# Kernel tuning notes

Measured on AMD Instinct MI355X. Metric: run time of the kernel, lower is better.

## Reference

```python
import jax, jax.numpy as jnp
import numpy as np

B, N, M, U, L = 2048, 256, 128, 512, 2   # batch, memory locations, memory width, num_units, num_layers
RH, WH, SH = 2, 2, 1                      # read heads, write heads, conv_shift_range
CLIP = 20.0
HEAD_R = M + 3 + (2 * SH + 1)             # 134 = k(M)+beta+g+s(2r+1)+gamma
HEAD_W = HEAD_R + 2 * M                   # 390 = + erase(M) + add(M)


def setup_inputs():
    key = jax.random.key(0)
    ks = jax.random.split(key, 12)
    def nrm(k, shape, s=0.05):
        return jax.random.normal(k, shape, jnp.float32) * s
    return {
        "X": jax.random.normal(ks[0], (B, U), jnp.float32),
        "m0": nrm(ks[1], (1, N, M), 0.5),
        "H0": nrm(ks[2], (L, 1, U)),
        "C0": nrm(ks[3], (L, 1, U)),
        "R0": nrm(ks[4], (RH, 1, M)),
        "A0": nrm(ks[5], (RH + WH, 1, N)),
        "W_prep": nrm(ks[6], (M * RH, U)),
        "b_prep": jnp.zeros((U,), jnp.float32),
        "W_lstm": nrm(ks[7], (L, 3 * U, 4 * U)),
        "b_lstm": jnp.zeros((L, 4 * U), jnp.float32),
        "W_r": nrm(ks[8], (U, RH * HEAD_R)),
        "b_r": jnp.zeros((RH * HEAD_R,), jnp.float32),
        "W_w": nrm(ks[9], (U, WH * HEAD_W)),
        "b_w": jnp.zeros((WH * HEAD_W,), jnp.float32),
        "W_ou": nrm(ks[10], (U + RH * M, U)),
        "b_ou": jnp.zeros((U,), jnp.float32),
    }


def _addressing(k, beta, g, s, gamma, m, a_prev):
    # k [B,M], beta/g/gamma [B], s [B,2*SH+1], m [B,N,M], a_prev [B,N]
    inner = jnp.einsum('bnm,bm->bn', m, k)
    k_norm = jnp.sqrt(jnp.sum(k * k, axis=1, keepdims=True))   # [B,1]
    m_norm = jnp.sqrt(jnp.sum(m * m, axis=2))                  # [B,N]
    K = inner / (k_norm * m_norm + 1e-8)
    w_c = jax.nn.softmax(beta[:, None] * K, axis=1)            # exp/sum in source == softmax
    w_g = g[:, None] * w_c + (1.0 - g[:, None]) * a_prev
    # The stacked-slice s_matrix in the source is exactly circular convolution:
    # w_conv[i] = sum_d s_d * w_g[(i - d) mod N], d in {0..SH, -SH..-1} matching s layout.
    shifts = list(range(0, SH + 1)) + list(range(-SH, 0))
    w_conv = sum(s[:, j:j + 1] * jnp.roll(w_g, shifts[j], axis=1) for j in range(2 * SH + 1))
    w_sharp = w_conv ** gamma[:, None]
    return w_sharp / jnp.sum(w_sharp, axis=1, keepdims=True)


def reference(X, m0, H0, C0, R0, A0, W_prep, b_prep, W_lstm, b_lstm,
              W_r, b_r, W_w, b_w, W_ou, b_ou):
    b = X.shape[0]
    m = jnp.broadcast_to(m0, (b, N, M))
    R_prev = [jnp.broadcast_to(jnp.tanh(R0[i]), (b, M)) for i in range(RH)]
    A_prev = [jnp.broadcast_to(jax.nn.softmax(A0[i], axis=-1), (b, N)) for i in range(RH + WH)]

    # controller
    h = jnp.concatenate(R_prev, axis=1) @ W_prep + b_prep
    for l in range(L):
        x_in = jnp.concatenate([X, h], axis=1)                              # [B,2U]
        h_prev = jnp.broadcast_to(H0[l], (b, U))
        c_prev = jnp.broadcast_to(C0[l], (b, U))
        z = jnp.concatenate([x_in, h_prev], axis=1) @ W_lstm[l] + b_lstm[l]  # [B,4U]
        i_g, f_g, g_g, o_g = jnp.split(z, 4, axis=1)
        c = jax.nn.sigmoid(f_g) * c_prev + jax.nn.sigmoid(i_g) * jnp.tanh(g_g)
        h = jax.nn.sigmoid(o_g) * jnp.tanh(c)
    h = jnp.clip(h, -CLIP, CLIP)

    r_heads = (h @ W_r + b_r).reshape(b, RH, HEAD_R)
    w_heads = (h @ W_w + b_w).reshape(b, WH, HEAD_W)
    heads = [r_heads[:, i] for i in range(RH)] + [w_heads[:, i] for i in range(WH)]

    A_t = []
    for ii, hd in enumerate(heads):
        A_t.append(_addressing(
            k=jnp.tanh(hd[:, :M]),
            beta=jax.nn.softplus(hd[:, M]),
            g=jax.nn.sigmoid(hd[:, M + 1]),
            s=jax.nn.softmax(hd[:, M + 2:M + 2 + 2 * SH + 1], axis=-1),
            gamma=jax.nn.softplus(hd[:, M + 2 + 2 * SH + 1]),
            m=m, a_prev=A_prev[ii]))

    # reads from old memory
    R_t = [jnp.einsum('bn,bnm->bm', A_t[i], m) for i in range(RH)]

    # sequential erase/add writes
    m_t = m
    for ii in range(WH):
        w = A_t[RH + ii][:, :, None]                                  # [B,N,1]
        del_v = jax.nn.sigmoid(w_heads[:, ii, -2 * M:-M])[:, None, :]  # [B,1,M]
        add_v = jnp.tanh(w_heads[:, ii, -M:])[:, None, :]
        m_t = m_t * (1.0 - w * del_v) + w * add_v

    y = jnp.clip(jnp.concatenate([h] + R_t, axis=1) @ W_ou + b_ou, -CLIP, CLIP)
    return y, m_t
```

## Files before the change

### kernel.cpp

```cpp
#include <hip/hip_runtime.h>
#include <math.h>

static constexpr int Bn = 2048;
static constexpr int Nn = 256;
static constexpr int Mn = 128;
static constexpr int Un = 512;

static constexpr size_t OFF_MNORM = 4608;
static constexpr size_t OFF_APREV = 4864;
static constexpr size_t OFF_BIASH = 5888;
static constexpr size_t OFF_KMAT  = 16384;
static constexpr size_t OFF_HEADS = OFF_KMAT + (size_t)8192 * 256;
static constexpr size_t OFF_AT    = OFF_HEADS + (size_t)2048 * 1048;
static constexpr size_t OFF_ERA   = OFF_AT + (size_t)2 * 2048 * 256;
static constexpr size_t OFF_ADD   = OFF_ERA + (size_t)2048 * 256;
static constexpr size_t OFF_XHB   = OFF_ADD + (size_t)2048 * 256;
static constexpr size_t OFF_HCAT  = OFF_XHB + 524288;
static constexpr size_t OFF_W0T   = OFF_HCAT + 524288;
static constexpr size_t OFF_W1T   = OFF_W0T + 524288;
static constexpr size_t OFF_WRWT  = OFF_W1T + 1048576;
static constexpr size_t OFF_WCOMB = OFF_WRWT + 294912;
static constexpr size_t OFF_WR2T  = OFF_WCOMB + 262144;
static constexpr size_t OFF_M0B   = OFF_WR2T + 65536;
static constexpr size_t OFF_ZPART = OFF_M0B + 16384 + 524288;

static constexpr int S_X0  = 0;
static constexpr int S_M0  = 512;
static constexpr int S_W0  = 528;
static constexpr int S_W1  = 1552;
static constexpr int S_WR  = 3600;
static constexpr int S_WW  = 3744;
static constexpr int S_WOU = 4144;
static constexpr int S_WR2 = 4400;
static constexpr int S_CA  = 4528;
static constexpr int S_ZC  = 4529;
static constexpr int S_END = 4657;

#define DEV __device__ __forceinline__

typedef __attribute__((ext_vector_type(8))) short bf16x8;
typedef __attribute__((ext_vector_type(4))) float f32x4;
typedef __attribute__((ext_vector_type(8))) unsigned short ushort8;
typedef unsigned int u32;

DEV float sigf(float x) { return 1.0f / (1.0f + expf(-x)); }
DEV float softplusf(float x) { return x > 20.0f ? x : log1pf(expf(x)); }
DEV unsigned short f2bf(float f) {
    unsigned u = __float_as_uint(f);
    u = (u + 0x7FFFu + ((u >> 16) & 1u)) >> 16;
    return (unsigned short)u;
}
DEV void gload16(const unsigned short* g, unsigned short* l) {
    __builtin_amdgcn_global_load_lds(
        (const __attribute__((address_space(1))) u32*)g,
        (__attribute__((address_space(3))) u32*)l, 16, 0, 0);
}

DEV float blk_reduce_max(float v, float* red) {
    int tid = threadIdx.x;
    red[tid] = v; __syncthreads();
    for (int s = (int)blockDim.x >> 1; s > 0; s >>= 1) {
        if (tid < s) red[tid] = fmaxf(red[tid], red[tid + s]);
        __syncthreads();
    }
    float r = red[0]; __syncthreads();
    return r;
}
DEV float blk_reduce_sum(float v, float* red) {
    int tid = threadIdx.x;
    red[tid] = v; __syncthreads();
    for (int s = (int)blockDim.x >> 1; s > 0; s >>= 1) {
        if (tid < s) red[tid] += red[tid + s];
        __syncthreads();
    }
    float r = red[0]; __syncthreads();
    return r;
}

#define GEMM_STAGE(buf, k0)                                                     \
    {                                                                           \
        _Pragma("unroll")                                                       \
        for (int q = 0; q < 2; ++q)                                             \
            gload16(A  + (size_t)(row0 + q * 32 + (tid >> 3)) * lda + (k0) + ke,\
                    &As[buf][q * 2048 + tid * 8]);                              \
        _Pragma("unroll")                                                       \
        for (int q = 0; q < 4; ++q)                                             \
            gload16(Wt + (size_t)(col0 + q * 32 + (tid >> 3)) * ldw + (k0) + ke,\
                    &Ws[buf][q * 2048 + tid * 8]);                              \
    }

#define GEMM_PROLOG                                                             \
    __shared__ __align__(16) unsigned short As[2][64 * 64];                     \
    __shared__ __align__(16) unsigned short Ws[2][128 * 64];                    \
    const int tid  = threadIdx.x;                                               \
    const int lane = tid & 63;                                                  \
    const int wave = tid >> 6;                                                  \
    const int wr = wave >> 1, wc = wave & 1;                                    \
    const int row0 = blockIdx.x * 64;                                           \
    const int col0 = blockIdx.y * 128;                                          \
    const int ke = ((tid & 7) * 8) ^ (((tid >> 3) & 7) << 3);                   \
    const int frow = lane & 15;                                                 \
    const int fko  = (lane >> 4) * 8;                                           \
    const int fxm  = (frow & 7) << 3;                                           \
    f32x4 acc[2][4];                                                            \
    _Pragma("unroll")                                                           \
    for (int i = 0; i < 2; ++i)                                                 \
        _Pragma("unroll")                                                       \
        for (int j = 0; j < 4; ++j) acc[i][j] = (f32x4){0.f, 0.f, 0.f, 0.f};

#define GEMM_FRAGS_AND_MFMA(Ab, Wb)                                             \
    {                                                                           \
        bf16x8 af[2][2], wf[2][4];                                              \
        _Pragma("unroll")                                                       \
        for (int kk = 0; kk < 2; ++kk) {                                        \
            _Pragma("unroll")                                                   \
            for (int i = 0; i < 2; ++i) {                                       \
                int fr = wr * 32 + i * 16 + frow;                               \
                af[kk][i] = *(const bf16x8*)&(Ab)[fr * 64 + ((kk * 32 + fko) ^ fxm)]; \
            }                                                                   \
            _Pragma("unroll")                                                   \
            for (int j = 0; j < 4; ++j) {                                       \
                int fr = wc * 64 + j * 16 + frow;                               \
                wf[kk][j] = *(const bf16x8*)&(Wb)[fr * 64 + ((kk * 32 + fko) ^ fxm)]; \
            }                                                                   \
        }                                                                       \
        __builtin_amdgcn_s_setprio(1);                                          \
        _Pragma("unroll")                                                       \
        for (int kk = 0; kk < 2; ++kk)                                          \
            _Pragma("unroll")                                                   \
            for (int i = 0; i < 2; ++i)                                         \
                _Pragma("unroll")                                               \
                for (int j = 0; j < 4; ++j)                                     \
                    acc[i][j] = __builtin_amdgcn_mfma_f32_16x16x32_bf16(        \
                        af[kk][i], wf[kk][j], acc[i][j], 0, 0, 0);              \
        __builtin_amdgcn_s_setprio(0);                                          \
    }

#define GEMM_MAINLOOP(Kr)                                                       \
    {                                                                           \
        const int nt = (Kr) >> 6;                                               \
        int cur = 0;                                                            \
        GEMM_STAGE(0, 0);                                                       \
        for (int t = 0; t < nt; ++t) {                                          \
            __syncthreads();                                                    \
            if (t + 1 < nt) GEMM_STAGE(cur ^ 1, (t + 1) * 64);                  \
            GEMM_FRAGS_AND_MFMA(As[cur], Ws[cur]);                              \
            cur ^= 1;                                                           \
        }                                                                       \
    }

__global__ __launch_bounds__(256) void gemm_bf16(
    const unsigned short* __restrict__ A, int lda,
    const unsigned short* __restrict__ Wt, int ldw,
    const float* __restrict__ bias,
    float* __restrict__ C, unsigned short* __restrict__ Cb, int ldc,
    int Nr, int Kr, int epi)
{
    GEMM_PROLOG
    GEMM_MAINLOOP(Kr)
    #pragma unroll
    for (int i = 0; i < 2; ++i) {
        int m0r = row0 + wr * 32 + i * 16 + (lane >> 4) * 4;
        #pragma unroll
        for (int j = 0; j < 4; ++j) {
            int n = col0 + wc * 64 + j * 16 + (lane & 15);
            if (n >= Nr) continue;
            float bv = bias ? bias[n] : 0.f;
            #pragma unroll
            for (int r = 0; r < 4; ++r) {
                float v = acc[i][j][r] + bv;
                if (epi == 1) v = fminf(fmaxf(v, -20.f), 20.f);
                if (epi == 2) Cb[(size_t)(m0r + r) * ldc + n] = f2bf(v);
                else          C [(size_t)(m0r + r) * ldc + n] = v;
            }
        }
    }
}

__global__ __launch_bounds__(256) void gemm_pfold(
    const unsigned short* __restrict__ WR2T,
    const unsigned short* __restrict__ M0B,
    unsigned short* __restrict__ WCOMB)
{
    const unsigned short* A  = WR2T + blockIdx.z * 128;
    const unsigned short* Wt = M0B;
    const int lda = 256, ldw = 128;
    unsigned short* Cb = WCOMB + 512 + blockIdx.z * 256;
    GEMM_PROLOG
    GEMM_MAINLOOP(128)
    #pragma unroll
    for (int i = 0; i < 2; ++i) {
        int m0r = row0 + wr * 32 + i * 16 + (lane >> 4) * 4;
        #pragma unroll
        for (int j = 0; j < 4; ++j) {
            int n = col0 + wc * 64 + j * 16 + (lane & 15);
            #pragma unroll
            for (int r = 0; r < 4; ++r)
                Cb[(size_t)(m0r + r) * 1024 + n] = f2bf(acc[i][j][r]);
        }
    }
}

__global__ __launch_bounds__(256) void gemm_lstm(
    const unsigned short* __restrict__ A, int lda,
    const unsigned short* __restrict__ Wt, int ldw,
    const float* __restrict__ zpart, const float* __restrict__ b_lstm,
    int z, const float* __restrict__ c0,
    unsigned short* __restrict__ hout, int ldh, int Kr, int doclip)
{
    GEMM_PROLOG
    GEMM_MAINLOOP(Kr)
    const int uu = lane & 15;
    const int q  = (col0 >> 6) + wc;
    const int uq = q * 16 + uu;
    const float c0v = c0[uq];
    float bg[4];
    #pragma unroll
    for (int g = 0; g < 4; ++g) {
        int j = g * 512 + q * 16 + uu;
        float a = b_lstm[z * 2048 + j];
        #pragma unroll
        for (int p = 0; p < 8; ++p)
            a += zpart[((size_t)z * 8 + p) * 2048 + j];
        bg[g] = a;
    }
    #pragma unroll
    for (int i = 0; i < 2; ++i) {
        int rbase = row0 + wr * 32 + i * 16 + (lane >> 4) * 4;
        #pragma unroll
        for (int r = 0; r < 4; ++r) {
            float ig = acc[i][0][r] + bg[0];
            float fg = acc[i][1][r] + bg[1];
            float gg = acc[i][2][r] + bg[2];
            float og = acc[i][3][r] + bg[3];
            float c = sigf(fg) * c0v + sigf(ig) * tanhf(gg);
            float h = sigf(og) * tanhf(c);
            if (doclip) h = fminf(fmaxf(h, -20.f), 20.f);
            hout[(size_t)(rbase + r) * ldh + uq] = f2bf(h);
        }
    }
}

__global__ __launch_bounds__(256) void gemm_kmat(
    const float* __restrict__ heads,
    const unsigned short* __restrict__ M0B,
    float* __restrict__ C)
{
    __shared__ __align__(16) unsigned short As[2][64 * 64];
    __shared__ __align__(16) unsigned short Ws[2][128 * 64];
    const int tid  = threadIdx.x;
    const int lane = tid & 63;
    const int wave = tid >> 6;
    const int wr = wave >> 1, wc = wave & 1;
    const int row0 = blockIdx.x * 64;
    const int col0 = blockIdx.y * 128;
    const int ke = ((tid & 7) * 8) ^ (((tid >> 3) & 7) << 3);
    const int frow = lane & 15;
    const int fko  = (lane >> 4) * 8;
    const int fxm  = (frow & 7) << 3;
    f32x4 acc[2][4];
    #pragma unroll
    for (int i = 0; i < 2; ++i)
        #pragma unroll
        for (int j = 0; j < 4; ++j) acc[i][j] = (f32x4){0.f, 0.f, 0.f, 0.f};

#define KMAT_STAGE(buf, k0)                                                     \
    {                                                                           \
        _Pragma("unroll")                                                       \
        for (int q = 0; q < 2; ++q) {                                           \
            int R = row0 + q * 32 + (tid >> 3);                                 \
            int b = R >> 2, ih = R & 3;                                         \
            int cb = (ih < 2) ? ih * 134 : 268 + (ih - 2) * 390;                \
            const float* hp = heads + (size_t)b * 1048 + cb + (k0) + ke;        \
            ushort8 o;                                                          \
            _Pragma("unroll")                                                   \
            for (int j = 0; j < 8; ++j) o[j] = f2bf(tanhf(hp[j]));              \
            *(ushort8*)&As[buf][q * 2048 + tid * 8] = o;                        \
        }                                                                       \
        _Pragma("unroll")                                                       \
        for (int q = 0; q < 4; ++q)                                             \
            gload16(M0B + (size_t)(col0 + q * 32 + (tid >> 3)) * 128 + (k0) + ke,\
                    &Ws[buf][q * 2048 + tid * 8]);                              \
    }

    int cur = 0;
    KMAT_STAGE(0, 0);
    for (int t = 0; t < 2; ++t) {
        __syncthreads();
        if (t == 0) KMAT_STAGE(1, 64);
        GEMM_FRAGS_AND_MFMA(As[cur], Ws[cur]);
        cur ^= 1;
    }
#undef KMAT_STAGE
    #pragma unroll
    for (int i = 0; i < 2; ++i) {
        int m0r = row0 + wr * 32 + i * 16 + (lane >> 4) * 4;
        #pragma unroll
        for (int j = 0; j < 4; ++j) {
            int n = col0 + wc * 64 + j * 16 + (lane & 15);
            #pragma unroll
            for (int r = 0; r < 4; ++r)
                C[(size_t)(m0r + r) * 256 + n] = acc[i][j][r];
        }
    }
}

DEV void dev_cvt8(const float* src, int lds, unsigned short* dst, int ldd,
                  int c8, int bloc, int tid)
{
    size_t idx = (size_t)bloc * 256 + tid;
    size_t r = idx / c8, c = (idx % c8) * 8;
    const float* s = src + r * lds + c;
    float4 v0 = *(const float4*)s;
    float4 v1 = *(const float4*)(s + 4);
    ushort8 o;
    o[0] = f2bf(v0.x); o[1] = f2bf(v0.y); o[2] = f2bf(v0.z); o[3] = f2bf(v0.w);
    o[4] = f2bf(v1.x); o[5] = f2bf(v1.y); o[6] = f2bf(v1.z); o[7] = f2bf(v1.w);
    *(ushort8*)(dst + r * ldd + c) = o;
}

DEV void dev_cvtT(const float* src, int R, int C, int lds,
                  unsigned short* dst, int ldd, int mode, int bx, int by,
                  int tid, float* t )
{
    const int x = tid & 31;
    for (int y = tid >> 5; y < 32; y += 8) {
        int r = by * 32 + y, c = bx * 32 + x;
        int scol = c;
        if (mode) scol = ((c >> 4) & 3) * 512 + (c >> 6) * 16 + (c & 15);
        t[y * 33 + x] = (r < R && c < C) ? src[(size_t)r * lds + scol] : 0.f;
    }
    __syncthreads();
    for (int y = tid >> 5; y < 32; y += 8) {
        int c = bx * 32 + y, r = by * 32 + x;
        if (c < C && r < R) dst[(size_t)c * ldd + r] = f2bf(t[x * 33 + y]);
    }
}

__global__ __launch_bounds__(256) void k_prep(
    const float* __restrict__ X, const float* __restrict__ m0,
    const float* __restrict__ H0, const float* __restrict__ R0,
    const float* __restrict__ A0, const float* __restrict__ W_prep,
    const float* __restrict__ b_prep, const float* __restrict__ W_lstm,
    const float* __restrict__ W_r, const float* __restrict__ b_r,
    const float* __restrict__ W_w, const float* __restrict__ b_w,
    const float* __restrict__ W_ou, float* __restrict__ ws)
{
    __shared__ float sh[32 * 33 + 64];
    const int bid = blockIdx.x, tid = threadIdx.x;
    unsigned short* XHB   = (unsigned short*)(ws + OFF_XHB);
    unsigned short* W0T   = (unsigned short*)(ws + OFF_W0T);
    unsigned short* W1T   = (unsigned short*)(ws + OFF_W1T);
    unsigned short* WRWT  = (unsigned short*)(ws + OFF_WRWT);
    unsigned short* WCOMB = (unsigned short*)(ws + OFF_WCOMB);
    unsigned short* WR2T  = (unsigned short*)(ws + OFF_WR2T);
    unsigned short* M0B   = (unsigned short*)(ws + OFF_M0B);

    if (bid < S_M0) {
        dev_cvt8(X, 512, XHB, 1024, 64, bid - S_X0, tid);
    } else if (bid < S_W0) {
        dev_cvt8(m0, 128, M0B, 128, 16, bid - S_M0, tid);
    } else if (bid < S_W1) {
        int s = bid - S_W0;
        dev_cvtT(W_lstm, 512, 2048, 2048, W0T, 512, 1, s & 63, s >> 6, tid, sh);
    } else if (bid < S_WR) {
        int s = bid - S_W1;
        dev_cvtT(W_lstm + (size_t)1536 * 2048, 1024, 2048, 2048, W1T, 1024, 1,
                 s & 63, s >> 6, tid, sh);
    } else if (bid < S_WW) {
        int s = bid - S_WR;
        dev_cvtT(W_r, 512, 268, 268, WRWT, 512, 0, s % 9, s / 9, tid, sh);
    } else if (bid < S_WOU) {
        int s = bid - S_WW;
        dev_cvtT(W_w, 512, 780, 780, WRWT + (size_t)268 * 512, 512, 0,
                 s % 25, s / 25, tid, sh);
    } else if (bid < S_WR2) {
        int s = bid - S_WOU;
        dev_cvtT(W_ou, 512, 512, 512, WCOMB, 1024, 0, s & 15, s >> 4, tid, sh);
    } else if (bid < S_CA) {
        int s = bid - S_WR2;
        dev_cvtT(W_ou + (size_t)512 * 512, 256, 512, 512, WR2T, 256, 0,
                 s & 15, s >> 4, tid, sh);
    } else if (bid < S_ZC) {
        float* red = sh;
        for (int i = 0; i < 4; ++i) {
            float v = A0[i * 256 + tid];
            float mx = blk_reduce_max(v, red);
            float e = expf(v - mx);
            float s = blk_reduce_sum(e, red);
            ws[OFF_APREV + i * 256 + tid] = e / s;
        }
        float acc = 0.f;
        for (int m = 0; m < 128; ++m) {
            float t = m0[(size_t)tid * 128 + m];
            acc = fmaf(t, t, acc);
        }
        ws[OFF_MNORM + tid] = sqrtf(acc);
        for (int j = tid; j < 1152; j += 256)
            ws[OFF_BIASH + j] = (j < 268) ? b_r[j] : (j < 1048 ? b_w[j - 268] : 0.f);
    } else {
        int sub = bid - S_ZC;
        int colb = sub & 7, up = (sub >> 3) & 7, z = sub >> 6;
        int j = colb * 256 + tid;
        float acc = 0.f;
        if (z == 0) {
            if (up < 4) {
                sh[256 + tid] = tanhf(R0[tid]);
                __syncthreads();
                if (tid < 128) {
                    int u = up * 128 + tid;
                    float a = b_prep[u];
                    for (int k = 0; k < 256; ++k)
                        a = fmaf(sh[256 + k], W_prep[(size_t)k * 512 + u], a);
                    sh[tid] = a;
                }
                __syncthreads();
                const int u0 = up * 128;
                #pragma unroll 4
                for (int t = 0; t < 128; ++t)
                    acc = fmaf(sh[t], W_lstm[(size_t)(512 + u0 + t) * 2048 + j], acc);
            } else {
                const int u0 = up * 128;
                #pragma unroll 4
                for (int t = 0; t < 128; ++t)
                    acc = fmaf(H0[u0 - 512 + t],
                               W_lstm[(size_t)(512 + u0 + t) * 2048 + j], acc);
            }
        } else {
            const int u0 = up * 64;
            const float* W1 = W_lstm + (size_t)1536 * 2048;
            #pragma unroll 4
            for (int t = 0; t < 64; ++t)
                acc = fmaf(H0[512 + u0 + t], W1[(size_t)(1024 + u0 + t) * 2048 + j], acc);
        }
        (ws + OFF_ZPART)[((size_t)z * 8 + up) * 2048 + j] = acc;
    }
}

__global__ __launch_bounds__(256) void k_addr(
    const float* __restrict__ heads, const float* __restrict__ kmat,
    const float* __restrict__ mnorm, const float* __restrict__ aprev,
    float* __restrict__ at, unsigned short* __restrict__ hcat,
    float* __restrict__ era, float* __restrict__ addv)
{
    __shared__ float red[256];
    __shared__ float wgs[256];
    __shared__ float sc[6];
    const int b = blockIdx.x, i = blockIdx.y, tid = threadIdx.x;
    const int cb = (i < 2) ? i * 134 : 268 + (i - 2) * 390;
    const float* hd = heads + (size_t)b * 1048 + cb;
    float kv = (tid < 128) ? tanhf(hd[tid]) : 0.f;
    float ksq = blk_reduce_sum(kv * kv, red);
    float kn = sqrtf(ksq);
    if (i >= 2 && tid < 128) {
        era [((size_t)b * 2 + (i - 2)) * 128 + tid] = sigf(hd[134 + tid]);
        addv[((size_t)b * 2 + (i - 2)) * 128 + tid] = tanhf(hd[262 + tid]);
    }
    if (tid == 0) {
        sc[0] = softplusf(hd[128]);
        sc[1] = sigf(hd[129]);
        float v0 = hd[130], v1 = hd[131], v2 = hd[132];
        float mx = fmaxf(v0, fmaxf(v1, v2));
        float e0 = expf(v0 - mx), e1 = expf(v1 - mx), e2 = expf(v2 - mx);
        float ssum = e0 + e1 + e2;
        sc[2] = e0 / ssum; sc[3] = e1 / ssum; sc[4] = e2 / ssum;
        sc[5] = softplusf(hd[133]);
    }
    __syncthreads();
    const float beta = sc[0], g = sc[1], s0 = sc[2], s1 = sc[3], s2 = sc[4],
                gamma = sc[5];
    float inner = kmat[((size_t)b * 4 + i) * 256 + tid];
    float K = inner / (kn * mnorm[tid] + 1e-8f);
    float x = beta * K;
    float mx = blk_reduce_max(x, red);
    float e = expf(x - mx);
    float se = blk_reduce_sum(e, red);
    float wc = e / se;
    float wg = g * wc + (1.f - g) * aprev[i * 256 + tid];
    wgs[tid] = wg;
    __syncthreads();
    float wconv = s0 * wg + s1 * wgs[(tid + 255) & 255] + s2 * wgs[(tid + 1) & 255];
    float wsh = powf(wconv, gamma);
    float ssum = blk_reduce_sum(wsh, red);
    float w = wsh / ssum;
    if (i < 2) hcat[(size_t)b * 1024 + 512 + i * 256 + tid] = f2bf(w);
    else       at[((size_t)(i - 2) * Bn + b) * 256 + tid] = w;
}

__global__ void k_mem(const float* __restrict__ m0, const float* __restrict__ at,
                      const float* __restrict__ era, const float* __restrict__ addv,
                      float* __restrict__ outm)
{
    const size_t total = (size_t)Bn * Nn * (Mn / 4);
    for (size_t idx = (size_t)blockIdx.x * blockDim.x + threadIdx.x;
         idx < total; idx += (size_t)gridDim.x * blockDim.x) {
        int mq = (int)(idx & 31);
        int n  = (int)((idx >> 5) & 255);
        int b  = (int)(idx >> 13);
        float4 t  = reinterpret_cast<const float4*>(m0)[n * 32 + mq];
        float w0 = at[((size_t)0 * Bn + b) * 256 + n];
        float w1 = at[((size_t)1 * Bn + b) * 256 + n];
        float4 e0 = reinterpret_cast<const float4*>(era) [((size_t)b * 2 + 0) * 32 + mq];
        float4 a0 = reinterpret_cast<const float4*>(addv)[((size_t)b * 2 + 0) * 32 + mq];
        float4 e1 = reinterpret_cast<const float4*>(era) [((size_t)b * 2 + 1) * 32 + mq];
        float4 a1 = reinterpret_cast<const float4*>(addv)[((size_t)b * 2 + 1) * 32 + mq];
#define UPD(c) { t.c = t.c * (1.f - w0 * e0.c) + w0 * a0.c; \
                 t.c = t.c * (1.f - w1 * e1.c) + w1 * a1.c; }
        UPD(x) UPD(y) UPD(z) UPD(w)
#undef UPD
        reinterpret_cast<float4*>(outm)[idx] = t;
    }
}

extern "C" void kernel_launch(void* const* d_in, const int* in_sizes, int n_in,
                              void* d_out, int out_size, void* d_ws, size_t ws_size,
                              hipStream_t stream)
{
    const float* X      = (const float*)d_in[0];
    const float* m0     = (const float*)d_in[1];
    const float* H0     = (const float*)d_in[2];
    const float* C0     = (const float*)d_in[3];
    const float* R0     = (const float*)d_in[4];
    const float* A0     = (const float*)d_in[5];
    const float* W_prep = (const float*)d_in[6];
    const float* b_prep = (const float*)d_in[7];
    const float* W_lstm = (const float*)d_in[8];
    const float* b_lstm = (const float*)d_in[9];
    const float* W_r    = (const float*)d_in[10];
    const float* b_r    = (const float*)d_in[11];
    const float* W_w    = (const float*)d_in[12];
    const float* b_w    = (const float*)d_in[13];
    const float* W_ou   = (const float*)d_in[14];
    const float* b_ou   = (const float*)d_in[15];
    float* ws  = (float*)d_ws;
    float* out = (float*)d_out;

    unsigned short* XHB   = (unsigned short*)(ws + OFF_XHB);
    unsigned short* HCAT  = (unsigned short*)(ws + OFF_HCAT);
    unsigned short* W0T   = (unsigned short*)(ws + OFF_W0T);
    unsigned short* W1T   = (unsigned short*)(ws + OFF_W1T);
    unsigned short* WRWT  = (unsigned short*)(ws + OFF_WRWT);
    unsigned short* WCOMB = (unsigned short*)(ws + OFF_WCOMB);
    unsigned short* WR2T  = (unsigned short*)(ws + OFF_WR2T);
    unsigned short* M0B   = (unsigned short*)(ws + OFF_M0B);

    k_prep<<<S_END, 256, 0, stream>>>(
        X, m0, H0, R0, A0, W_prep, b_prep, W_lstm, W_r, b_r, W_w, b_w, W_ou, ws);

    gemm_pfold<<<dim3(8, 2, 2), 256, 0, stream>>>(WR2T, M0B, WCOMB);

    gemm_lstm<<<dim3(32, 16), 256, 0, stream>>>(
        XHB, 1024, W0T, 512, ws + OFF_ZPART, b_lstm, 0, C0, XHB + 512, 1024, 512, 0);
    gemm_lstm<<<dim3(32, 16), 256, 0, stream>>>(
        XHB, 1024, W1T, 1024, ws + OFF_ZPART, b_lstm, 1, C0 + 512, HCAT, 1024, 1024, 1);

    gemm_bf16<<<dim3(32, 9), 256, 0, stream>>>(
        HCAT, 1024, WRWT, 512, ws + OFF_BIASH, ws + OFF_HEADS, nullptr, 1048, 1048, 512, 0);

    gemm_kmat<<<dim3(128, 2), 256, 0, stream>>>(
        ws + OFF_HEADS, M0B, ws + OFF_KMAT);

    k_addr<<<dim3(Bn, 4), 256, 0, stream>>>(
        ws + OFF_HEADS, ws + OFF_KMAT, ws + OFF_MNORM, ws + OFF_APREV,
        ws + OFF_AT, HCAT, ws + OFF_ERA, ws + OFF_ADD);

    gemm_bf16<<<dim3(32, 4), 256, 0, stream>>>(
        HCAT, 1024, WCOMB, 1024, b_ou, out, nullptr, 512, 512, 1024, 1);

    k_mem<<<2048, 256, 0, stream>>>(
        m0, ws + OFF_AT, ws + OFF_ERA, ws + OFF_ADD, out + (size_t)Bn * Un);
}
```

Measured before the change: 205.7 us.

## Fuse write-head addressing into memory update kernel and rework GEMM barriers

The write-head addressing (erase/add vectors and attention weights) now runs inside the memory-update kernel, one block per batch row, and the results stay in shared memory. This removes the global round trip for at/era/add and shrinks k_addr to the two read heads. The GEMM main loop also swaps its single __syncthreads for explicit vmcnt waits and two s_barriers per iteration, so the next tile's global loads can stay in flight during the MFMA work. In exchange, the memory-update blocks do a serial addressing phase before streaming, and the extra barrier adds sync cost.

```diff
diff --git a/kernel.cpp b/kernel.cpp
--- a/kernel.cpp
+++ b/kernel.cpp
@@ -11,10 +11,7 @@
 static constexpr size_t OFF_BIASH = 5888;
 static constexpr size_t OFF_KMAT  = 16384;
 static constexpr size_t OFF_HEADS = OFF_KMAT + (size_t)8192 * 256;
-static constexpr size_t OFF_AT    = OFF_HEADS + (size_t)2048 * 1048;
-static constexpr size_t OFF_ERA   = OFF_AT + (size_t)2 * 2048 * 256;
-static constexpr size_t OFF_ADD   = OFF_ERA + (size_t)2048 * 256;
-static constexpr size_t OFF_XHB   = OFF_ADD + (size_t)2048 * 256;
+static constexpr size_t OFF_XHB   = OFF_HEADS + (size_t)2048 * 1048;
 static constexpr size_t OFF_HCAT  = OFF_XHB + 524288;
 static constexpr size_t OFF_W0T   = OFF_HCAT + 524288;
 static constexpr size_t OFF_W1T   = OFF_W0T + 524288;
@@ -142,9 +139,18 @@
         int cur = 0;                                                            \
         GEMM_STAGE(0, 0);                                                       \
         for (int t = 0; t < nt; ++t) {                                          \
-            __syncthreads();                                                    \
-            if (t + 1 < nt) GEMM_STAGE(cur ^ 1, (t + 1) * 64);                  \
+            if (t + 1 < nt) {                                                   \
+                GEMM_STAGE(cur ^ 1, (t + 1) * 64);                              \
+                asm volatile("s_waitcnt vmcnt(6)" ::: "memory");                \
+            } else {                                                            \
+                asm volatile("s_waitcnt vmcnt(0)" ::: "memory");                \
+            }                                                                   \
+            __builtin_amdgcn_sched_barrier(0);                                  \
+            __builtin_amdgcn_s_barrier();                                       \
+            __builtin_amdgcn_sched_barrier(0);                                  \
             GEMM_FRAGS_AND_MFMA(As[cur], Ws[cur]);                              \
+            __builtin_amdgcn_sched_barrier(0);                                  \
+            __builtin_amdgcn_s_barrier();                                       \
             cur ^= 1;                                                           \
         }                                                                       \
     }
@@ -440,22 +446,15 @@
 __global__ __launch_bounds__(256) void k_addr(
     const float* __restrict__ heads, const float* __restrict__ kmat,
     const float* __restrict__ mnorm, const float* __restrict__ aprev,
-    float* __restrict__ at, unsigned short* __restrict__ hcat,
-    float* __restrict__ era, float* __restrict__ addv)
+    unsigned short* __restrict__ hcat)
 {
     __shared__ float red[256];
     __shared__ float wgs[256];
     __shared__ float sc[6];
     const int b = blockIdx.x, i = blockIdx.y, tid = threadIdx.x;
-    const int cb = (i < 2) ? i * 134 : 268 + (i - 2) * 390;
-    const float* hd = heads + (size_t)b * 1048 + cb;
+    const float* hd = heads + (size_t)b * 1048 + i * 134;
     float kv = (tid < 128) ? tanhf(hd[tid]) : 0.f;
-    float ksq = blk_reduce_sum(kv * kv, red);
-    float kn = sqrtf(ksq);
-    if (i >= 2 && tid < 128) {
-        era [((size_t)b * 2 + (i - 2)) * 128 + tid] = sigf(hd[134 + tid]);
-        addv[((size_t)b * 2 + (i - 2)) * 128 + tid] = tanhf(hd[262 + tid]);
-    }
+    float kn = sqrtf(blk_reduce_sum(kv * kv, red));
     if (tid == 0) {
         sc[0] = softplusf(hd[128]);
         sc[1] = sigf(hd[129]);
@@ -482,33 +481,76 @@
     float wconv = s0 * wg + s1 * wgs[(tid + 255) & 255] + s2 * wgs[(tid + 1) & 255];
     float wsh = powf(wconv, gamma);
     float ssum = blk_reduce_sum(wsh, red);
-    float w = wsh / ssum;
-    if (i < 2) hcat[(size_t)b * 1024 + 512 + i * 256 + tid] = f2bf(w);
-    else       at[((size_t)(i - 2) * Bn + b) * 256 + tid] = w;
-}
-
-__global__ void k_mem(const float* __restrict__ m0, const float* __restrict__ at,
-                      const float* __restrict__ era, const float* __restrict__ addv,
-                      float* __restrict__ outm)
-{
-    const size_t total = (size_t)Bn * Nn * (Mn / 4);
-    for (size_t idx = (size_t)blockIdx.x * blockDim.x + threadIdx.x;
-         idx < total; idx += (size_t)gridDim.x * blockDim.x) {
-        int mq = (int)(idx & 31);
-        int n  = (int)((idx >> 5) & 255);
-        int b  = (int)(idx >> 13);
-        float4 t  = reinterpret_cast<const float4*>(m0)[n * 32 + mq];
-        float w0 = at[((size_t)0 * Bn + b) * 256 + n];
-        float w1 = at[((size_t)1 * Bn + b) * 256 + n];
-        float4 e0 = reinterpret_cast<const float4*>(era) [((size_t)b * 2 + 0) * 32 + mq];
-        float4 a0 = reinterpret_cast<const float4*>(addv)[((size_t)b * 2 + 0) * 32 + mq];
-        float4 e1 = reinterpret_cast<const float4*>(era) [((size_t)b * 2 + 1) * 32 + mq];
-        float4 a1 = reinterpret_cast<const float4*>(addv)[((size_t)b * 2 + 1) * 32 + mq];
+    hcat[(size_t)b * 1024 + 512 + i * 256 + tid] = f2bf(wsh / ssum);
+}
+
+__global__ __launch_bounds__(256) void k_mem(
+    const float* __restrict__ m0, const float* __restrict__ heads,
+    const float* __restrict__ kmat, const float* __restrict__ mnorm,
+    const float* __restrict__ aprev, float* __restrict__ outm)
+{
+    __shared__ float red[256];
+    __shared__ float wgs[256];
+    __shared__ float sc[6];
+    __shared__ __align__(16) float at_s[2][256];
+    __shared__ __align__(16) float er_s[2][128];
+    __shared__ __align__(16) float ad_s[2][128];
+    const int b = blockIdx.x, tid = threadIdx.x;
+
+    for (int ii = 0; ii < 2; ++ii) {
+        const int i = 2 + ii;
+        const float* hd = heads + (size_t)b * 1048 + 268 + ii * 390;
+        float kv = (tid < 128) ? tanhf(hd[tid]) : 0.f;
+        float kn = sqrtf(blk_reduce_sum(kv * kv, red));
+        if (tid < 128) {
+            er_s[ii][tid] = sigf(hd[134 + tid]);
+            ad_s[ii][tid] = tanhf(hd[262 + tid]);
+        }
+        if (tid == 0) {
+            sc[0] = softplusf(hd[128]);
+            sc[1] = sigf(hd[129]);
+            float v0 = hd[130], v1 = hd[131], v2 = hd[132];
+            float mx = fmaxf(v0, fmaxf(v1, v2));
+            float e0 = expf(v0 - mx), e1 = expf(v1 - mx), e2 = expf(v2 - mx);
+            float ssum = e0 + e1 + e2;
+            sc[2] = e0 / ssum; sc[3] = e1 / ssum; sc[4] = e2 / ssum;
+            sc[5] = softplusf(hd[133]);
+        }
+        __syncthreads();
+        const float beta = sc[0], g = sc[1], s0 = sc[2], s1 = sc[3],
+                    s2 = sc[4], gamma = sc[5];
+        float inner = kmat[((size_t)b * 4 + i) * 256 + tid];
+        float K = inner / (kn * mnorm[tid] + 1e-8f);
+        float x = beta * K;
+        float mx = blk_reduce_max(x, red);
+        float e = expf(x - mx);
+        float se = blk_reduce_sum(e, red);
+        float wc = e / se;
+        float wg = g * wc + (1.f - g) * aprev[i * 256 + tid];
+        wgs[tid] = wg;
+        __syncthreads();
+        float wconv = s0 * wg + s1 * wgs[(tid + 255) & 255] + s2 * wgs[(tid + 1) & 255];
+        float wsh = powf(wconv, gamma);
+        float ssum = blk_reduce_sum(wsh, red);
+        at_s[ii][tid] = wsh / ssum;
+        __syncthreads();
+    }
+
+    const float4* m0v = (const float4*)m0;
+    float4* outv = (float4*)outm + (size_t)b * 8192;
+    for (int idx = tid; idx < 8192; idx += 256) {
+        int mq = idx & 31, n = idx >> 5;
+        float4 t = m0v[n * 32 + mq];
+        float w0 = at_s[0][n], w1 = at_s[1][n];
+        float4 e0 = *(const float4*)&er_s[0][mq * 4];
+        float4 a0 = *(const float4*)&ad_s[0][mq * 4];
+        float4 e1 = *(const float4*)&er_s[1][mq * 4];
+        float4 a1 = *(const float4*)&ad_s[1][mq * 4];
 #define UPD(c) { t.c = t.c * (1.f - w0 * e0.c) + w0 * a0.c; \
                  t.c = t.c * (1.f - w1 * e1.c) + w1 * a1.c; }
         UPD(x) UPD(y) UPD(z) UPD(w)
 #undef UPD
-        reinterpret_cast<float4*>(outm)[idx] = t;
+        outv[idx] = t;
     }
 }
 
@@ -560,13 +602,13 @@
     gemm_kmat<<<dim3(128, 2), 256, 0, stream>>>(
         ws + OFF_HEADS, M0B, ws + OFF_KMAT);
 
-    k_addr<<<dim3(Bn, 4), 256, 0, stream>>>(
-        ws + OFF_HEADS, ws + OFF_KMAT, ws + OFF_MNORM, ws + OFF_APREV,
-        ws + OFF_AT, HCAT, ws + OFF_ERA, ws + OFF_ADD);
+    k_addr<<<dim3(Bn, 2), 256, 0, stream>>>(
+        ws + OFF_HEADS, ws + OFF_KMAT, ws + OFF_MNORM, ws + OFF_APREV, HCAT);
 
     gemm_bf16<<<dim3(32, 4), 256, 0, stream>>>(
         HCAT, 1024, WCOMB, 1024, b_ou, out, nullptr, 512, 512, 1024, 1);
 
-    k_mem<<<2048, 256, 0, stream>>>(
-        m0, ws + OFF_AT, ws + OFF_ERA, ws + OFF_ADD, out + (size_t)Bn * Un);
-}
+    k_mem<<<Bn, 256, 0, stream>>>(
+        m0, ws + OFF_HEADS, ws + OFF_KMAT, ws + OFF_MNORM, ws + OFF_APREV,
+        out + (size_t)Bn * Un);
+}
```

New measurement: 202.8 us. No clear change (-1.4%).
